# Optimization experiments

Hardware: AMD Instinct MI355X
Metric: run time of the kernel (lower is better)

## Reference

```python
import jax, jax.numpy as jnp
import numpy as np

N_NODES = 100000
N_EDGES = 1600000
IN_F = 128
HID = 128
N_CLASSES = 2
N_GRAPHS = 512


def setup_inputs() -> dict:
    key = jax.random.key(0)
    ks = jax.random.split(key, 12)
    x = jax.random.normal(ks[0], (N_NODES, IN_F), dtype=jnp.float32)
    edge_index = jax.random.randint(ks[1], (2, N_EDGES), 0, N_NODES, dtype=jnp.int64)
    batch = jnp.sort(jax.random.randint(ks[2], (N_NODES,), 0, N_GRAPHS, dtype=jnp.int64))
    s_in = 1.0 / np.sqrt(IN_F)
    s_h = 1.0 / np.sqrt(HID)
    return {
        "x": x,
        "edge_index": edge_index,
        "batch": batch,
        "W1": jax.random.normal(ks[3], (IN_F, HID), dtype=jnp.float32) * s_in,
        "b1": jnp.zeros((HID,), dtype=jnp.float32),
        "W2": jax.random.normal(ks[4], (HID, HID), dtype=jnp.float32) * s_h,
        "b2": jnp.zeros((HID,), dtype=jnp.float32),
        "W3": jax.random.normal(ks[5], (HID, HID), dtype=jnp.float32) * s_h,
        "b3": jnp.zeros((HID,), dtype=jnp.float32),
        "Wl": jax.random.normal(ks[6], (HID, N_CLASSES), dtype=jnp.float32) * s_h,
        "bl": jnp.zeros((N_CLASSES,), dtype=jnp.float32),
    }


def reference(x, edge_index, batch, W1, b1, W2, b2, W3, b3, Wl, bl):
    n = x.shape[0]
    src, dst = edge_index[0], edge_index[1]
    # GCNConv adds self-loops and applies symmetric normalization D^-1/2 (A+I) D^-1/2
    loop = jnp.arange(n, dtype=src.dtype)
    src_f = jnp.concatenate([src, loop])  # [E+N]
    dst_f = jnp.concatenate([dst, loop])
    deg = jax.ops.segment_sum(jnp.ones_like(src_f, dtype=x.dtype), dst_f, num_segments=n)
    dis = jax.lax.rsqrt(jnp.maximum(deg, 1.0))  # deg >= 1 due to self-loops
    norm = dis[src_f] * dis[dst_f]  # [E+N]

    def conv(h, W, b):
        h = h @ W                                    # [N, H]
        msg = h[src_f] * norm[:, None]               # gather + scale  [E+N, H]
        agg = jax.ops.segment_sum(msg, dst_f, num_segments=n)  # scatter-add
        return agg + b

    h = jax.nn.relu(conv(x, W1, b1))
    h = jax.nn.relu(conv(h, W2, b2))
    h = conv(h, W3, b3)
    # global_mean_pool over graph ids
    sums = jax.ops.segment_sum(h, batch, num_segments=N_GRAPHS)        # [G, H]
    cnt = jax.ops.segment_sum(jnp.ones((n,), h.dtype), batch, num_segments=N_GRAPHS)
    pooled = sums / jnp.maximum(cnt, 1.0)[:, None]
    # dropout p=0.5 is identity in eval mode
    return pooled @ Wl + bl
```

## Files before the change

kernel.cpp:

```cpp
#include <hip/hip_runtime.h>

#define NF 128
#define NFU 64
#define BW 128
#define KMAX 1024
#define CAP 3072
#define CHUNK 8192

typedef __attribute__((ext_vector_type(8))) short bf16x8;
typedef __attribute__((ext_vector_type(4))) float f32x4;
typedef __attribute__((ext_vector_type(2))) float f32x2;
union U4S8 { uint4 u; bf16x8 s; };

__device__ inline unsigned pack_bf16(float a, float b) {
    unsigned ua = __float_as_uint(a), ub = __float_as_uint(b);
    ua = (ua + 0x7fffu + ((ua >> 16) & 1u)) >> 16;
    ub = (ub + 0x7fffu + ((ub >> 16) & 1u)) >> 16;
    return ua | (ub << 16);
}
__device__ inline float bflo(unsigned u) { return __uint_as_float(u << 16); }
__device__ inline float bfhi(unsigned u) { return __uint_as_float(u & 0xFFFF0000u); }

__global__ void detect_init_kernel(const int* __restrict__ ei, int ne, int* __restrict__ mode,
                                   int* __restrict__ gcur, int K, float* __restrict__ out, int osz) {
    if (blockIdx.x == 0) {
        if (threadIdx.x == 0) {
            int step = ne / 32; if (step < 1) step = 1;
            int all0 = 1;
            for (int k = 0; k < 16; ++k) {
                int idx = 2 * k * step + 1;
                if (ei[idx] != 0) { all0 = 0; break; }
            }
            *mode = all0;
        }
    } else {
        int i = (blockIdx.x - 1) * 256 + threadIdx.x;
        int stride = 8 * 256;
        for (int k = i; k < K; k += stride) gcur[k] = k * CAP;
        for (int k = i; k < osz; k += stride) out[k] = 0.f;
    }
}

__global__ __launch_bounds__(256) void wprep_gbounds_kernel(const float* __restrict__ W1, const float* __restrict__ W2,
                                                            const float* __restrict__ W3, uint4* __restrict__ Wb,
                                                            const int* __restrict__ batch, const int* __restrict__ mode,
                                                            int* __restrict__ gstart, int n, int G) {
    int tid = threadIdx.x;
    if (blockIdx.x < 3) {
        const float* W = (blockIdx.x == 0) ? W1 : (blockIdx.x == 1) ? W2 : W3;
        uint4* o = Wb + (size_t)blockIdx.x * 2048;
#pragma unroll
        for (int it = 0; it < 8; ++it) {
            int item = it * 256 + tid;
            int lane = item & 63;
            int kbjt = item >> 6;
            int kb = kbjt & 3, jt = kbjt >> 2;
            int k0 = kb * 32 + (lane >> 4) * 8;
            int j = jt * 16 + (lane & 15);
            unsigned p[4];
#pragma unroll
            for (int q = 0; q < 4; ++q)
                p[q] = pack_bf16(W[(size_t)(k0 + 2 * q) * NF + j], W[(size_t)(k0 + 2 * q + 1) * NF + j]);
            o[item] = make_uint4(p[0], p[1], p[2], p[3]);
        }
    } else {
        int m = *mode;
        int i = (blockIdx.x - 3) * 256 + tid;
        if (i >= n) return;
        int g1 = m ? batch[2 * i] : batch[i];
        int g2 = (i == n - 1) ? G : (m ? batch[2 * (i + 1)] : batch[i + 1]);
        if ((unsigned)g1 > (unsigned)G) g1 = G;
        if ((unsigned)g2 > (unsigned)G) g2 = G;
        if (i == 0) for (int g = 0; g <= g1; ++g) gstart[g] = 0;
        for (int g = g1 + 1; g <= g2; ++g) gstart[g] = i + 1;
    }
}

__global__ __launch_bounds__(256) void scatter_kernel(const int* __restrict__ ei, int ne, int n,
                                                      const int* __restrict__ mode, int* __restrict__ gcur,
                                                      unsigned* __restrict__ pairbuf, int K) {
    __shared__ int cur[KMAX];
    int m = *mode;
    int tid = threadIdx.x;
    for (int k = tid; k < K; k += 256) cur[k] = 0;
    __syncthreads();
    int base = blockIdx.x * CHUNK;
    int end = min(base + CHUNK, ne);
    for (int e = base + tid; e < end; e += 256) {
        int dst = m ? ei[2 * (ne + e)] : ei[ne + e];
        if ((unsigned)dst < (unsigned)n) atomicAdd(&cur[dst >> 7], 1);
    }
    __syncthreads();
    for (int k = tid; k < K; k += 256) {
        int c = cur[k];
        cur[k] = c ? atomicAdd(&gcur[k], c) : 0;
    }
    __syncthreads();
    for (int e = base + tid; e < end; e += 256) {
        int src = m ? ei[2 * e] : ei[e];
        int dst = m ? ei[2 * (ne + e)] : ei[ne + e];
        if ((unsigned)dst >= (unsigned)n || (unsigned)src >= (unsigned)n) continue;
        int b = dst >> 7;
        int pos = atomicAdd(&cur[b], 1);
        if (pos < (b + 1) * CAP)
            pairbuf[pos] = (unsigned)src | ((unsigned)(dst & (BW - 1)) << 24);
    }
}

__global__ __launch_bounds__(256) void sort_kernel(const unsigned* __restrict__ pairbuf,
                                                   const int* __restrict__ gcur,
                                                   int* __restrict__ rowstart, int* __restrict__ rowend,
                                                   float* __restrict__ dis,
                                                   int* __restrict__ col, int n, int K) {
    __shared__ unsigned spair[CAP];
    __shared__ int lcol[CAP];
    __shared__ int dcnt[BW];
    __shared__ int pref[BW];
    int tid = threadIdx.x;
    int b = blockIdx.x;
    int r0 = b * BW;
    int base = b * CAP;
    int cntb = gcur[b] - base;
    if (cntb > CAP) cntb = CAP;
    if (cntb < 0) cntb = 0;

    for (int i = tid; i < cntb; i += 256) spair[i] = pairbuf[base + i];
    if (tid < BW) dcnt[tid] = 0;
    __syncthreads();
    for (int i = tid; i < cntb; i += 256) atomicAdd(&dcnt[spair[i] >> 24], 1);
    __syncthreads();
    if (tid < BW) pref[tid] = dcnt[tid];
    __syncthreads();
    for (int off = 1; off < BW; off <<= 1) {
        int t = (tid < BW && tid >= off) ? pref[tid - off] : 0;
        __syncthreads();
        if (tid < BW) pref[tid] += t;
        __syncthreads();
    }
    if (tid < BW) {
        int d = r0 + tid;
        if (d < n) {
            int excl = pref[tid] - dcnt[tid];
            rowstart[d] = base + excl;
            rowend[d]   = base + pref[tid];
            dis[d] = rsqrtf((float)(dcnt[tid] + 1));
        }
    }
    if (tid < BW) dcnt[tid] = pref[tid] - dcnt[tid];
    __syncthreads();
    for (int i = tid; i < cntb; i += 256) {
        unsigned p = spair[i];
        int slot = atomicAdd(&dcnt[p >> 24], 1);
        if (slot < CAP) lcol[slot] = (int)(p & 0xFFFFFFu);
    }
    __syncthreads();
    for (int i = tid; i < cntb; i += 256) col[base + i] = lcol[i];
}

__global__ __launch_bounds__(256) void mm_mfma_kernel(const float* __restrict__ Af,
                                                      const uint4* __restrict__ Wb,
                                                      const float* __restrict__ dis,
                                                      unsigned* __restrict__ hs, int n) {
    int tid = threadIdx.x;
    int wave = tid >> 6, lane = tid & 63;
    int r0 = blockIdx.x * 64 + wave * 16;
    if (r0 >= n) return;
    int lrow = lane & 15, lk = lane >> 4;
    int arow = min(r0 + lrow, n - 1);

    f32x4 acc[8];
#pragma unroll
    for (int j = 0; j < 8; ++j) acc[j] = (f32x4){0.f, 0.f, 0.f, 0.f};

    U4S8 af[4];
#pragma unroll
    for (int kb = 0; kb < 4; ++kb) {
        const float* p = Af + (size_t)arow * NF + kb * 32 + lk * 8;
        float4 x0 = *(const float4*)p;
        float4 x1 = *(const float4*)(p + 4);
        af[kb].u = make_uint4(pack_bf16(x0.x, x0.y), pack_bf16(x0.z, x0.w),
                              pack_bf16(x1.x, x1.y), pack_bf16(x1.z, x1.w));
    }

#pragma unroll
    for (int kb = 0; kb < 4; ++kb) {
#pragma unroll
        for (int jt = 0; jt < 8; ++jt) {
            U4S8 wf;
            wf.u = Wb[(jt * 4 + kb) * 64 + lane];
            acc[jt] = __builtin_amdgcn_mfma_f32_16x16x32_bf16(wf.s, af[kb].s, acc[jt], 0, 0, 0);
        }
    }

    if (r0 + lrow < n) {
        float dv = dis[r0 + lrow];
        unsigned* orow = hs + (size_t)(r0 + lrow) * NFU;
#pragma unroll
        for (int jt = 0; jt < 8; ++jt) {
            unsigned p0 = pack_bf16(acc[jt][0] * dv, acc[jt][1] * dv);
            unsigned p1 = pack_bf16(acc[jt][2] * dv, acc[jt][3] * dv);
            *(uint2*)(orow + jt * 8 + lk * 2) = make_uint2(p0, p1);
        }
    }
}

#define SPACC(v)                                              \
    { a0 += (f32x2){bflo((v).x), bfhi((v).x)};                \
      a1 += (f32x2){bflo((v).y), bfhi((v).y)};                \
      a2 += (f32x2){bflo((v).z), bfhi((v).z)};                \
      a3 += (f32x2){bflo((v).w), bfhi((v).w)}; }

__device__ inline void gather_row(const unsigned* __restrict__ hsf, const int* __restrict__ col,
                                  int s, int e, int row, int fl, int gbase,
                                  f32x2& a0, f32x2& a1, f32x2& a2, f32x2& a3) {
    uint4 sv = *(const uint4*)(hsf + (size_t)row * NFU);
    a0 = (f32x2){bflo(sv.x), bfhi(sv.x)};
    a1 = (f32x2){bflo(sv.y), bfhi(sv.y)};
    a2 = (f32x2){bflo(sv.z), bfhi(sv.z)};
    a3 = (f32x2){bflo(sv.w), bfhi(sv.w)};
    int deg = e - s;
    for (int jb = 0; jb < deg; jb += 16) {
        int m = min(16, deg - jb);
        int cidx = col[s + jb + ((fl < m) ? fl : (m - 1))];
        int j = 0;
        for (; j + 4 <= m; j += 4) {
            int c0 = __shfl(cidx, gbase + j);
            int c1 = __shfl(cidx, gbase + j + 1);
            int c2 = __shfl(cidx, gbase + j + 2);
            int c3 = __shfl(cidx, gbase + j + 3);
            uint4 v0 = *(const uint4*)(hsf + (size_t)c0 * NFU);
            uint4 v1 = *(const uint4*)(hsf + (size_t)c1 * NFU);
            uint4 v2 = *(const uint4*)(hsf + (size_t)c2 * NFU);
            uint4 v3 = *(const uint4*)(hsf + (size_t)c3 * NFU);
            SPACC(v0); SPACC(v1); SPACC(v2); SPACC(v3);
        }
        for (; j < m; ++j) {
            int c0 = __shfl(cidx, gbase + j);
            uint4 v0 = *(const uint4*)(hsf + (size_t)c0 * NFU);
            SPACC(v0);
        }
    }
}

__global__ __launch_bounds__(256) void spmm_kernel(const unsigned* __restrict__ hs,
                                                   const int* __restrict__ rowstart, const int* __restrict__ rowend,
                                                   const int* __restrict__ col, const float* __restrict__ dis,
                                                   const float* __restrict__ b, unsigned* __restrict__ outb,
                                                   int n) {
    int row = (blockIdx.x * blockDim.x + threadIdx.x) >> 4;
    int fl = threadIdx.x & 15;
    int gbase = threadIdx.x & 48;
    if (row >= n) return;
    int s = rowstart[row], e = rowend[row];
    const unsigned* hsf = hs + fl * 4;
    f32x2 a0, a1, a2, a3;
    gather_row(hsf, col, s, e, row, fl, gbase, a0, a1, a2, a3);

    float d = dis[row];
    float4 bb0 = *(const float4*)(b + fl * 8);
    float4 bb1 = *(const float4*)(b + fl * 8 + 4);
    float o[8];
    o[0] = fmaf(d, a0[0], bb0.x); o[1] = fmaf(d, a0[1], bb0.y);
    o[2] = fmaf(d, a1[0], bb0.z); o[3] = fmaf(d, a1[1], bb0.w);
    o[4] = fmaf(d, a2[0], bb1.x); o[5] = fmaf(d, a2[1], bb1.y);
    o[6] = fmaf(d, a3[0], bb1.z); o[7] = fmaf(d, a3[1], bb1.w);
    unsigned q0 = pack_bf16(o[0], o[1]);
    unsigned q1 = pack_bf16(o[2], o[3]);
    unsigned q2 = pack_bf16(o[4], o[5]);
    unsigned q3 = pack_bf16(o[6], o[7]);
    *(uint4*)(outb + (size_t)row * NFU + fl * 4) = make_uint4(q0, q1, q2, q3);
}

__global__ __launch_bounds__(256) void spmm_mm_kernel(const unsigned* __restrict__ hs_in,
                                                      const int* __restrict__ rowstart, const int* __restrict__ rowend,
                                                      const int* __restrict__ col,
                                                      const float* __restrict__ dis, const float* __restrict__ b,
                                                      const uint4* __restrict__ Wb,
                                                      unsigned* __restrict__ hs_out, int n) {
    __shared__ unsigned lh[16][65];
    int tid = threadIdx.x;
    int rloc = tid >> 4;
    int row0 = blockIdx.x * 16;
    int row = row0 + rloc;
    int fl = tid & 15;
    int gbase = tid & 48;

    if (row < n) {
        int s = rowstart[row], e = rowend[row];
        const unsigned* hsf = hs_in + fl * 4;
        f32x2 a0, a1, a2, a3;
        gather_row(hsf, col, s, e, row, fl, gbase, a0, a1, a2, a3);

        float d = dis[row];
        float4 bb0 = *(const float4*)(b + fl * 8);
        float4 bb1 = *(const float4*)(b + fl * 8 + 4);
        float o[8];
        o[0] = fmaxf(fmaf(d, a0[0], bb0.x), 0.f); o[1] = fmaxf(fmaf(d, a0[1], bb0.y), 0.f);
        o[2] = fmaxf(fmaf(d, a1[0], bb0.z), 0.f); o[3] = fmaxf(fmaf(d, a1[1], bb0.w), 0.f);
        o[4] = fmaxf(fmaf(d, a2[0], bb1.x), 0.f); o[5] = fmaxf(fmaf(d, a2[1], bb1.y), 0.f);
        o[6] = fmaxf(fmaf(d, a3[0], bb1.z), 0.f); o[7] = fmaxf(fmaf(d, a3[1], bb1.w), 0.f);
        lh[rloc][fl * 4 + 0] = pack_bf16(o[0], o[1]);
        lh[rloc][fl * 4 + 1] = pack_bf16(o[2], o[3]);
        lh[rloc][fl * 4 + 2] = pack_bf16(o[4], o[5]);
        lh[rloc][fl * 4 + 3] = pack_bf16(o[6], o[7]);
    }
    __syncthreads();

    if (tid < 64) {
        int lane = tid;
        int lrow = lane & 15, lk = lane >> 4;
        f32x4 acc[8];
#pragma unroll
        for (int j = 0; j < 8; ++j) acc[j] = (f32x4){0.f, 0.f, 0.f, 0.f};
        U4S8 af[4];
#pragma unroll
        for (int kb = 0; kb < 4; ++kb) {
            unsigned* p = &lh[lrow][kb * 16 + lk * 4];
            af[kb].u = make_uint4(p[0], p[1], p[2], p[3]);
        }
#pragma unroll
        for (int kb = 0; kb < 4; ++kb) {
#pragma unroll
            for (int jt = 0; jt < 8; ++jt) {
                U4S8 wf;
                wf.u = Wb[(jt * 4 + kb) * 64 + lane];
                acc[jt] = __builtin_amdgcn_mfma_f32_16x16x32_bf16(wf.s, af[kb].s, acc[jt], 0, 0, 0);
            }
        }
        int orow_i = row0 + lrow;
        if (orow_i < n) {
            float dv = dis[orow_i];
            unsigned* orow = hs_out + (size_t)orow_i * NFU;
#pragma unroll
            for (int jt = 0; jt < 8; ++jt) {
                unsigned p0 = pack_bf16(acc[jt][0] * dv, acc[jt][1] * dv);
                unsigned p1 = pack_bf16(acc[jt][2] * dv, acc[jt][3] * dv);
                *(uint2*)(orow + jt * 8 + lk * 2) = make_uint2(p0, p1);
            }
        }
    }
}

__global__ __launch_bounds__(256) void poolhead_kernel(const unsigned* __restrict__ h, const int* __restrict__ gstart,
                                                       const float* __restrict__ Wl, const float* __restrict__ bl,
                                                       float* __restrict__ out, int G) {
    __shared__ float sacc[16][16][8];
    int g = blockIdx.x >> 2, sub = blockIdx.x & 3;
    int s0 = gstart[g], e0 = gstart[g + 1];
    int cnt = e0 - s0;
    int per = (cnt + 3) >> 2;
    int s = s0 + sub * per;
    int e = min(s + per, e0);
    int tid = threadIdx.x;
    int rg = tid >> 4, fl = tid & 15;

    float acc[8] = {0.f, 0.f, 0.f, 0.f, 0.f, 0.f, 0.f, 0.f};
    for (int i = s + rg; i < e; i += 16) {
        uint4 v = *(const uint4*)(h + (size_t)i * NFU + fl * 4);
        acc[0] += bflo(v.x); acc[1] += bfhi(v.x);
        acc[2] += bflo(v.y); acc[3] += bfhi(v.y);
        acc[4] += bflo(v.z); acc[5] += bfhi(v.z);
        acc[6] += bflo(v.w); acc[7] += bfhi(v.w);
    }
#pragma unroll
    for (int k = 0; k < 8; ++k) sacc[rg][fl][k] = acc[k];
    __syncthreads();
    if (tid < 16) {
        float t[8] = {0.f, 0.f, 0.f, 0.f, 0.f, 0.f, 0.f, 0.f};
        for (int r = 0; r < 16; ++r)
#pragma unroll
            for (int k = 0; k < 8; ++k) t[k] += sacc[r][tid][k];
        float inv = 1.0f / fmaxf((float)cnt, 1.0f);
        float o0 = 0.f, o1 = 0.f;
#pragma unroll
        for (int k = 0; k < 8; ++k) {
            int f = tid * 8 + k;
            o0 += t[k] * inv * Wl[f * 2];
            o1 += t[k] * inv * Wl[f * 2 + 1];
        }
#pragma unroll
        for (int off2 = 8; off2; off2 >>= 1) {
            o0 += __shfl_down(o0, off2, 16);
            o1 += __shfl_down(o1, off2, 16);
        }
        if (tid == 0) {
            if (sub == 0) { o0 += bl[0]; o1 += bl[1]; }
            atomicAdd(&out[g * 2 + 0], o0);
            atomicAdd(&out[g * 2 + 1], o1);
        }
    }
}

extern "C" void kernel_launch(void* const* d_in, const int* in_sizes, int n_in,
                              void* d_out, int out_size, void* d_ws, size_t ws_size,
                              hipStream_t stream) {
    const float* x  = (const float*)d_in[0];
    const int*   ei = (const int*)d_in[1];
    const int*   bt = (const int*)d_in[2];
    const float* W1 = (const float*)d_in[3];
    const float* b1 = (const float*)d_in[4];
    const float* W2 = (const float*)d_in[5];
    const float* b2 = (const float*)d_in[6];
    const float* W3 = (const float*)d_in[7];
    const float* b3 = (const float*)d_in[8];
    const float* Wl = (const float*)d_in[9];
    const float* bl = (const float*)d_in[10];
    float* out = (float*)d_out;

    const int n  = in_sizes[2];
    const int ne = in_sizes[1] / 2;
    const int G  = out_size / 2;
    const int K  = (n + BW - 1) / BW;
    const int nchunks = (ne + CHUNK - 1) / CHUNK;

    size_t off = 0;
    auto alloc = [&](size_t bytes) { size_t o = off; off += (bytes + 255) & ~(size_t)255; return o; };
    char* ws = (char*)d_ws;
    unsigned* hsA     = (unsigned*)(ws + alloc((size_t)n * NFU * 4));
    unsigned* hsB     = (unsigned*)(ws + alloc((size_t)n * NFU * 4));
    unsigned* h3      = (unsigned*)(ws + alloc((size_t)n * NFU * 4));
    unsigned* pairbuf = (unsigned*)(ws + alloc((size_t)K * CAP * 4));
    int*      col     = (int*)     (ws + alloc((size_t)K * CAP * 4));
    int*      rowstart= (int*)     (ws + alloc((size_t)n * 4));
    int*      rowend  = (int*)     (ws + alloc((size_t)n * 4));
    float*    dis     = (float*)   (ws + alloc((size_t)n * 4));
    int*      gcur    = (int*)     (ws + alloc((size_t)(K + 1) * 4));
    int*      gstart  = (int*)     (ws + alloc((size_t)(G + 1) * 4));
    uint4*    Wb      = (uint4*)   (ws + alloc(3 * 2048 * 16));
    int*      mode    = (int*)     (ws + alloc(256));
    (void)ws_size;

    detect_init_kernel<<<9, 256, 0, stream>>>(ei, ne, mode, gcur, K, out, out_size);
    wprep_gbounds_kernel<<<3 + (n + 255) / 256, 256, 0, stream>>>(W1, W2, W3, Wb, bt, mode, gstart, n, G);

    scatter_kernel<<<nchunks, 256, 0, stream>>>(ei, ne, n, mode, gcur, pairbuf, K);
    sort_kernel<<<K, 256, 0, stream>>>(pairbuf, gcur, rowstart, rowend, dis, col, n, K);

    const int mm_grid = (n + 63) / 64;
    const int sp_grid = (n + 15) / 16;

    mm_mfma_kernel<<<mm_grid, 256, 0, stream>>>(x, Wb, dis, hsA, n);
    spmm_mm_kernel<<<sp_grid, 256, 0, stream>>>(hsA, rowstart, rowend, col, dis, b1, Wb + 2048, hsB, n);
    spmm_mm_kernel<<<sp_grid, 256, 0, stream>>>(hsB, rowstart, rowend, col, dis, b2, Wb + 4096, hsA, n);
    spmm_kernel<<<sp_grid, 256, 0, stream>>>(hsA, rowstart, rowend, col, dis, b3, h3, n);

    poolhead_kernel<<<G * 4, 256, 0, stream>>>(h3, gstart, Wl, bl, out, G);
}
```

Baseline: 279.9 us.

## Merge prep kernels, split MFMA across all waves, widen pooling grid

Folds the mode-detect/init kernel into the weight-prep/graph-bounds kernel, saving one launch; each block recomputes the layout mode locally instead of reading it from memory. In the fused SpMM+matmul kernel the 16x128 MFMA epilogue is now spread over all four waves, two output tiles each, instead of running on one wave while the other three sit idle. Out-of-range rows are zero-filled in shared memory. The pooling kernel uses 8 sub-blocks per graph instead of 4, raising parallelism at the cost of more atomics on the output.

```diff
diff --git a/kernel.cpp b/kernel.cpp
--- a/kernel.cpp
+++ b/kernel.cpp
@@ -21,30 +21,23 @@
 __device__ inline float bflo(unsigned u) { return __uint_as_float(u << 16); }
 __device__ inline float bfhi(unsigned u) { return __uint_as_float(u & 0xFFFF0000u); }
 
-__global__ void detect_init_kernel(const int* __restrict__ ei, int ne, int* __restrict__ mode,
-                                   int* __restrict__ gcur, int K, float* __restrict__ out, int osz) {
-    if (blockIdx.x == 0) {
-        if (threadIdx.x == 0) {
-            int step = ne / 32; if (step < 1) step = 1;
-            int all0 = 1;
-            for (int k = 0; k < 16; ++k) {
-                int idx = 2 * k * step + 1;
-                if (ei[idx] != 0) { all0 = 0; break; }
-            }
-            *mode = all0;
-        }
-    } else {
-        int i = (blockIdx.x - 1) * 256 + threadIdx.x;
-        int stride = 8 * 256;
-        for (int k = i; k < K; k += stride) gcur[k] = k * CAP;
-        for (int k = i; k < osz; k += stride) out[k] = 0.f;
-    }
-}
-
-__global__ __launch_bounds__(256) void wprep_gbounds_kernel(const float* __restrict__ W1, const float* __restrict__ W2,
-                                                            const float* __restrict__ W3, uint4* __restrict__ Wb,
-                                                            const int* __restrict__ batch, const int* __restrict__ mode,
-                                                            int* __restrict__ gstart, int n, int G) {
+__device__ inline int detect_mode(const int* __restrict__ ei, int ne) {
+    int step = ne / 32; if (step < 1) step = 1;
+    int all0 = 1;
+    for (int k = 0; k < 16; ++k) {
+        int idx = 2 * k * step + 1;
+        if (ei[idx] != 0) { all0 = 0; break; }
+    }
+    return all0;
+}
+
+__global__ __launch_bounds__(256) void prep_kernel(const float* __restrict__ W1, const float* __restrict__ W2,
+                                                   const float* __restrict__ W3, uint4* __restrict__ Wb,
+                                                   const int* __restrict__ ei, int ne,
+                                                   const int* __restrict__ batch, int* __restrict__ mode,
+                                                   int* __restrict__ gstart, int n, int G,
+                                                   int* __restrict__ gcur, int K,
+                                                   float* __restrict__ out, int osz, int nb) {
     int tid = threadIdx.x;
     if (blockIdx.x < 3) {
         const float* W = (blockIdx.x == 0) ? W1 : (blockIdx.x == 1) ? W2 : W3;
@@ -63,8 +56,8 @@
                 p[q] = pack_bf16(W[(size_t)(k0 + 2 * q) * NF + j], W[(size_t)(k0 + 2 * q + 1) * NF + j]);
             o[item] = make_uint4(p[0], p[1], p[2], p[3]);
         }
-    } else {
-        int m = *mode;
+    } else if (blockIdx.x < 3 + nb) {
+        int m = detect_mode(ei, ne);
         int i = (blockIdx.x - 3) * 256 + tid;
         if (i >= n) return;
         int g1 = m ? batch[2 * i] : batch[i];
@@ -73,6 +66,13 @@
         if ((unsigned)g2 > (unsigned)G) g2 = G;
         if (i == 0) for (int g = 0; g <= g1; ++g) gstart[g] = 0;
         for (int g = g1 + 1; g <= g2; ++g) gstart[g] = i + 1;
+    } else {
+        int bi = blockIdx.x - 3 - nb;
+        if (bi == 0 && tid == 0) *mode = detect_mode(ei, ne);
+        int i = bi * 256 + tid;
+        int stride = 8 * 256;
+        for (int k = i; k < K; k += stride) gcur[k] = k * CAP;
+        for (int k = i; k < osz; k += stride) out[k] = 0.f;
     }
 }
 
@@ -303,41 +303,41 @@
         lh[rloc][fl * 4 + 1] = pack_bf16(o[2], o[3]);
         lh[rloc][fl * 4 + 2] = pack_bf16(o[4], o[5]);
         lh[rloc][fl * 4 + 3] = pack_bf16(o[6], o[7]);
-    }
-    __syncthreads();
-
-    if (tid < 64) {
-        int lane = tid;
-        int lrow = lane & 15, lk = lane >> 4;
-        f32x4 acc[8];
-#pragma unroll
-        for (int j = 0; j < 8; ++j) acc[j] = (f32x4){0.f, 0.f, 0.f, 0.f};
-        U4S8 af[4];
-#pragma unroll
-        for (int kb = 0; kb < 4; ++kb) {
-            unsigned* p = &lh[lrow][kb * 16 + lk * 4];
-            af[kb].u = make_uint4(p[0], p[1], p[2], p[3]);
-        }
-#pragma unroll
-        for (int kb = 0; kb < 4; ++kb) {
-#pragma unroll
-            for (int jt = 0; jt < 8; ++jt) {
-                U4S8 wf;
-                wf.u = Wb[(jt * 4 + kb) * 64 + lane];
-                acc[jt] = __builtin_amdgcn_mfma_f32_16x16x32_bf16(wf.s, af[kb].s, acc[jt], 0, 0, 0);
-            }
-        }
-        int orow_i = row0 + lrow;
-        if (orow_i < n) {
-            float dv = dis[orow_i];
-            unsigned* orow = hs_out + (size_t)orow_i * NFU;
-#pragma unroll
-            for (int jt = 0; jt < 8; ++jt) {
-                unsigned p0 = pack_bf16(acc[jt][0] * dv, acc[jt][1] * dv);
-                unsigned p1 = pack_bf16(acc[jt][2] * dv, acc[jt][3] * dv);
-                *(uint2*)(orow + jt * 8 + lk * 2) = make_uint2(p0, p1);
-            }
-        }
+    } else {
+        lh[rloc][fl * 4 + 0] = 0; lh[rloc][fl * 4 + 1] = 0;
+        lh[rloc][fl * 4 + 2] = 0; lh[rloc][fl * 4 + 3] = 0;
+    }
+    __syncthreads();
+
+    int lane = tid & 63, wave = tid >> 6;
+    int lrow = lane & 15, lk = lane >> 4;
+    int jt0 = wave * 2;
+    f32x4 acc0 = (f32x4){0.f, 0.f, 0.f, 0.f};
+    f32x4 acc1 = (f32x4){0.f, 0.f, 0.f, 0.f};
+    U4S8 af[4];
+#pragma unroll
+    for (int kb = 0; kb < 4; ++kb) {
+        unsigned* p = &lh[lrow][kb * 16 + lk * 4];
+        af[kb].u = make_uint4(p[0], p[1], p[2], p[3]);
+    }
+#pragma unroll
+    for (int kb = 0; kb < 4; ++kb) {
+        U4S8 w0, w1;
+        w0.u = Wb[(jt0 * 4 + kb) * 64 + lane];
+        w1.u = Wb[((jt0 + 1) * 4 + kb) * 64 + lane];
+        acc0 = __builtin_amdgcn_mfma_f32_16x16x32_bf16(w0.s, af[kb].s, acc0, 0, 0, 0);
+        acc1 = __builtin_amdgcn_mfma_f32_16x16x32_bf16(w1.s, af[kb].s, acc1, 0, 0, 0);
+    }
+    int orow_i = row0 + lrow;
+    if (orow_i < n) {
+        float dv = dis[orow_i];
+        unsigned* orow = hs_out + (size_t)orow_i * NFU;
+        unsigned p0 = pack_bf16(acc0[0] * dv, acc0[1] * dv);
+        unsigned p1 = pack_bf16(acc0[2] * dv, acc0[3] * dv);
+        *(uint2*)(orow + jt0 * 8 + lk * 2) = make_uint2(p0, p1);
+        unsigned p2 = pack_bf16(acc1[0] * dv, acc1[1] * dv);
+        unsigned p3 = pack_bf16(acc1[2] * dv, acc1[3] * dv);
+        *(uint2*)(orow + (jt0 + 1) * 8 + lk * 2) = make_uint2(p2, p3);
     }
 }
 
@@ -345,10 +345,10 @@
                                                        const float* __restrict__ Wl, const float* __restrict__ bl,
                                                        float* __restrict__ out, int G) {
     __shared__ float sacc[16][16][8];
-    int g = blockIdx.x >> 2, sub = blockIdx.x & 3;
+    int g = blockIdx.x >> 3, sub = blockIdx.x & 7;
     int s0 = gstart[g], e0 = gstart[g + 1];
     int cnt = e0 - s0;
-    int per = (cnt + 3) >> 2;
+    int per = (cnt + 7) >> 3;
     int s = s0 + sub * per;
     int e = min(s + per, e0);
     int tid = threadIdx.x;
@@ -412,6 +412,7 @@
     const int G  = out_size / 2;
     const int K  = (n + BW - 1) / BW;
     const int nchunks = (ne + CHUNK - 1) / CHUNK;
+    const int nb = (n + 255) / 256;
 
     size_t off = 0;
     auto alloc = [&](size_t bytes) { size_t o = off; off += (bytes + 255) & ~(size_t)255; return o; };
@@ -430,8 +431,8 @@
     int*      mode    = (int*)     (ws + alloc(256));
     (void)ws_size;
 
-    detect_init_kernel<<<9, 256, 0, stream>>>(ei, ne, mode, gcur, K, out, out_size);
-    wprep_gbounds_kernel<<<3 + (n + 255) / 256, 256, 0, stream>>>(W1, W2, W3, Wb, bt, mode, gstart, n, G);
+    prep_kernel<<<3 + nb + 8, 256, 0, stream>>>(W1, W2, W3, Wb, ei, ne, bt, mode,
+                                                gstart, n, G, gcur, K, out, out_size, nb);
 
     scatter_kernel<<<nchunks, 256, 0, stream>>>(ei, ne, n, mode, gcur, pairbuf, K);
     sort_kernel<<<K, 256, 0, stream>>>(pairbuf, gcur, rowstart, rowend, dis, col, n, K);
@@ -444,5 +445,5 @@
     spmm_mm_kernel<<<sp_grid, 256, 0, stream>>>(hsB, rowstart, rowend, col, dis, b2, Wb + 4096, hsA, n);
     spmm_kernel<<<sp_grid, 256, 0, stream>>>(hsA, rowstart, rowend, col, dis, b3, h3, n);
 
-    poolhead_kernel<<<G * 4, 256, 0, stream>>>(h3, gstart, Wl, bl, out, G);
-}
+    poolhead_kernel<<<G * 8, 256, 0, stream>>>(h3, gstart, Wl, bl, out, G);
+}
```

After: 271.5 us. 1.03x faster.
